# Kernel optimization log

Hardware: AMD Instinct MI355X
Metric: run time of the kernel (lower is better)

The kernel has to match this reference:

```python
import math
import jax, jax.numpy as jnp
import numpy as np

B, T, D = 512, 512, 256
ALPHA = 0.5
BETA = 0.9


def setup_inputs() -> dict:
    key = jax.random.key(0)
    ks = jax.random.split(key, 9)
    s = 1.0 / math.sqrt(D)
    return {
        "window_features": jax.random.normal(ks[0], (B, T, D), jnp.float32),
        "timestamps": jax.random.uniform(ks[1], (B, T), jnp.float32) * 86400.0 * 7,
        "prev_L": jax.random.normal(ks[2], (B, D), jnp.float32),
        "prev_M": jax.random.uniform(ks[3], (B, 1), jnp.float32),
        "pad_mask": jnp.zeros((B, T), jnp.bool_),
        "W_Q": jax.random.normal(ks[4], (D, D), jnp.float32) * s,
        "W_K": jax.random.normal(ks[5], (D, D), jnp.float32) * s,
        "W_V": jax.random.normal(ks[6], (D, D), jnp.float32) * s,
        "cls_w": jax.random.normal(ks[7], (1, 2 * D + 1), jnp.float32) * s,
        "cls_b": jnp.zeros((1,), jnp.float32),
    }


def reference(window_features, timestamps, prev_L, prev_M, pad_mask,
              W_Q, W_K, W_V, cls_w, cls_b):
    Bv, Tv, d = window_features.shape
    valid = ~pad_mask
    valid_f = valid.astype(window_features.dtype)              # [B,T]
    valid_count = jnp.clip(valid_f.sum(1, keepdims=True), 1.0)  # [B,1]

    # decay weights from recency (days)
    t_masked = jnp.where(pad_mask, -1e18, timestamps)
    t_max = t_masked.max(1, keepdims=True)                      # [B,1]
    dt = jnp.clip(t_max - timestamps, 0.0) / 86400.0
    lam = jnp.exp(-ALPHA * dt) * valid_f                        # [B,T]

    # mean-pooled query
    q = (window_features * valid_f[..., None]).sum(1) / valid_count  # [B,d]
    Q = q @ W_Q.T                                               # [B,d]
    K = jnp.einsum('btd,ed->bte', window_features, W_K)         # [B,T,d]
    V = jnp.einsum('btd,ed->bte', window_features, W_V)         # [B,T,d]

    scores = jnp.einsum('bd,btd->bt', Q, K) / math.sqrt(d)      # [B,T]
    scores = jnp.where(pad_mask, -1e9, scores)
    attn = jax.nn.softmax(scores, axis=-1)

    # decay-modulated reweighting + renormalization
    w = lam * attn
    w = w / (w.sum(1, keepdims=True) + 1e-8)

    L_t = jnp.einsum('bt,btd->bd', w, V)                        # [B,d]
    delta_t = L_t - prev_L
    M_t = BETA * prev_M + (1.0 - BETA) * jnp.linalg.norm(delta_t, axis=1, keepdims=True)
    T_event = jnp.concatenate([L_t, delta_t, M_t], axis=-1)     # [B,2d+1]
    p = (T_event @ cls_w.T + cls_b).squeeze(-1)                 # [B]
    return (p, T_event, L_t, M_t)
```

## Files before the change

kernel.cpp:

```cpp
#include <hip/hip_runtime.h>
#include <math.h>

#define ALPHA 0.5f
#define BETA 0.9f
#define Bsz 512
#define Tsz 512
#define Dsz 256

__device__ __forceinline__ float wave_reduce_sum(float v) {
    v += __shfl_xor(v, 32, 64);
    v += __shfl_xor(v, 16, 64);
    v += __shfl_xor(v, 8, 64);
    v += __shfl_xor(v, 4, 64);
    v += __shfl_xor(v, 2, 64);
    v += __shfl_xor(v, 1, 64);
    return v;
}

__device__ __forceinline__ float wave_reduce_max(float v) {
    v = fmaxf(v, __shfl_xor(v, 32, 64));
    v = fmaxf(v, __shfl_xor(v, 16, 64));
    v = fmaxf(v, __shfl_xor(v, 8, 64));
    v = fmaxf(v, __shfl_xor(v, 4, 64));
    v = fmaxf(v, __shfl_xor(v, 2, 64));
    v = fmaxf(v, __shfl_xor(v, 1, 64));
    return v;
}

__global__ __launch_bounds__(256) void kA(const float* __restrict__ x,
                                          const float* __restrict__ ts,
                                          const unsigned char* __restrict__ pad,
                                          const float* __restrict__ WQ,
                                          const float* __restrict__ WK,
                                          float* __restrict__ qk,
                                          float* __restrict__ tmax_out) {
    const int b = blockIdx.x;
    const int tid = threadIdx.x;
    const int w = tid >> 6, lane = tid & 63;

    __shared__ float validS[Tsz];
    __shared__ float qpart[4][Dsz];
    __shared__ float qS[Dsz];
    __shared__ float QS[Dsz];
    __shared__ float red[8];
    __shared__ float tmaxS, cntS;

    float lmax = -1e30f;
    float lcnt = 0.f;
    for (int t = tid; t < Tsz; t += 256) {
        bool v = (pad[(size_t)b * Tsz + t] == 0);
        float tv = ts[(size_t)b * Tsz + t];
        validS[t] = v ? 1.f : 0.f;
        if (v) { lmax = fmaxf(lmax, tv); lcnt += 1.f; }
    }
    lmax = wave_reduce_max(lmax);
    lcnt = wave_reduce_sum(lcnt);
    if (lane == 0) { red[w] = lmax; red[4 + w] = lcnt; }
    __syncthreads();
    if (tid == 0) {
        tmaxS = fmaxf(fmaxf(red[0], red[1]), fmaxf(red[2], red[3]));
        cntS = fmaxf(red[4] + red[5] + red[6] + red[7], 1.f);
    }
    __syncthreads();

    const float* xb = x + (size_t)b * Tsz * Dsz;
    float4 a0 = make_float4(0.f, 0.f, 0.f, 0.f);
    float4 a1 = a0, a2 = a0, a3 = a0;
    const int tbase = w * 128;
    for (int i = 0; i < 128; i += 4) {
        const int t = tbase + i;
        float4 x0 = *(const float4*)(xb + (size_t)(t + 0) * Dsz + lane * 4);
        float4 x1 = *(const float4*)(xb + (size_t)(t + 1) * Dsz + lane * 4);
        float4 x2 = *(const float4*)(xb + (size_t)(t + 2) * Dsz + lane * 4);
        float4 x3 = *(const float4*)(xb + (size_t)(t + 3) * Dsz + lane * 4);
        const float v0 = validS[t], v1 = validS[t + 1], v2 = validS[t + 2], v3 = validS[t + 3];
        a0.x += v0 * x0.x; a0.y += v0 * x0.y; a0.z += v0 * x0.z; a0.w += v0 * x0.w;
        a1.x += v1 * x1.x; a1.y += v1 * x1.y; a1.z += v1 * x1.z; a1.w += v1 * x1.w;
        a2.x += v2 * x2.x; a2.y += v2 * x2.y; a2.z += v2 * x2.z; a2.w += v2 * x2.w;
        a3.x += v3 * x3.x; a3.y += v3 * x3.y; a3.z += v3 * x3.z; a3.w += v3 * x3.w;
    }
    float4 accq;
    accq.x = (a0.x + a1.x) + (a2.x + a3.x);
    accq.y = (a0.y + a1.y) + (a2.y + a3.y);
    accq.z = (a0.z + a1.z) + (a2.z + a3.z);
    accq.w = (a0.w + a1.w) + (a2.w + a3.w);
    qpart[w][lane * 4 + 0] = accq.x;
    qpart[w][lane * 4 + 1] = accq.y;
    qpart[w][lane * 4 + 2] = accq.z;
    qpart[w][lane * 4 + 3] = accq.w;
    __syncthreads();
    qS[tid] = (qpart[0][tid] + qpart[1][tid] + qpart[2][tid] + qpart[3][tid]) / cntS;
    __syncthreads();

    float Qi = 0.f;
    const float* wqrow = WQ + (size_t)tid * Dsz;
    #pragma unroll 4
    for (int d4 = 0; d4 < Dsz; d4 += 4) {
        float4 wv = *(const float4*)(wqrow + d4);
        Qi += wv.x * qS[d4] + wv.y * qS[d4 + 1] + wv.z * qS[d4 + 2] + wv.w * qS[d4 + 3];
    }
    QS[tid] = Qi;
    __syncthreads();

    float v = 0.f;
    #pragma unroll 8
    for (int e = 0; e < Dsz; ++e) {
        v += QS[e] * WK[(size_t)e * Dsz + tid];
    }
    qk[(size_t)b * Dsz + tid] = v * 0.0625f;
    if (tid == 0) tmax_out[b] = tmaxS;
}

__global__ __launch_bounds__(256) void kB(const float* __restrict__ x,
                                          const float* __restrict__ ts,
                                          const unsigned char* __restrict__ pad,
                                          const float* __restrict__ qk,
                                          const float* __restrict__ tmax_in,
                                          const float* __restrict__ WV,
                                          const float* __restrict__ prevL,
                                          const float* __restrict__ prevM,
                                          const float* __restrict__ clsw,
                                          const float* __restrict__ clsb,
                                          float* __restrict__ out) {
    const int b = blockIdx.x;
    const int tid = threadIdx.x;
    const int w = tid >> 6, lane = tid & 63;

    __shared__ float lamS[Tsz];
    __shared__ float okS[Tsz];
    __shared__ float accS[4][Dsz];
    __shared__ float EGS[8];
    __shared__ float xwS[Dsz];
    __shared__ float red[4];
    __shared__ float red2[4];

    const float tmax = tmax_in[b];
    for (int t = tid; t < Tsz; t += 256) {
        bool valid = (pad[(size_t)b * Tsz + t] == 0);
        float dt = fmaxf(tmax - ts[(size_t)b * Tsz + t], 0.f) * (1.f / 86400.f);
        lamS[t] = valid ? __expf(-ALPHA * dt) : 0.f;
        okS[t] = valid ? 1.f : 0.f;
    }
    __syncthreads();

    const float4 qk4 = *(const float4*)(qk + (size_t)b * Dsz + lane * 4);
    const float* xb = x + (size_t)b * Tsz * Dsz;
    float4 acc = make_float4(0.f, 0.f, 0.f, 0.f);
    float E = 0.f, G = 0.f;
    const int tbase = w * 128;
    for (int i = 0; i < 128; i += 4) {
        const int t = tbase + i;
        float4 x0 = *(const float4*)(xb + (size_t)(t + 0) * Dsz + lane * 4);
        float4 x1 = *(const float4*)(xb + (size_t)(t + 1) * Dsz + lane * 4);
        float4 x2 = *(const float4*)(xb + (size_t)(t + 2) * Dsz + lane * 4);
        float4 x3 = *(const float4*)(xb + (size_t)(t + 3) * Dsz + lane * 4);
        float s0 = qk4.x * x0.x + qk4.y * x0.y + qk4.z * x0.z + qk4.w * x0.w;
        float s1 = qk4.x * x1.x + qk4.y * x1.y + qk4.z * x1.z + qk4.w * x1.w;
        float s2 = qk4.x * x2.x + qk4.y * x2.y + qk4.z * x2.z + qk4.w * x2.w;
        float s3 = qk4.x * x3.x + qk4.y * x3.y + qk4.z * x3.z + qk4.w * x3.w;
        #pragma unroll
        for (int off = 32; off >= 1; off >>= 1) {
            s0 += __shfl_xor(s0, off, 64);
            s1 += __shfl_xor(s1, off, 64);
            s2 += __shfl_xor(s2, off, 64);
            s3 += __shfl_xor(s3, off, 64);
        }
        float e0 = okS[t + 0] * __expf(s0);
        float e1 = okS[t + 1] * __expf(s1);
        float e2 = okS[t + 2] * __expf(s2);
        float e3 = okS[t + 3] * __expf(s3);
        float g0 = lamS[t + 0] * e0;
        float g1 = lamS[t + 1] * e1;
        float g2 = lamS[t + 2] * e2;
        float g3 = lamS[t + 3] * e3;
        E += (e0 + e1) + (e2 + e3);
        G += (g0 + g1) + (g2 + g3);
        acc.x += g0 * x0.x + g1 * x1.x + g2 * x2.x + g3 * x3.x;
        acc.y += g0 * x0.y + g1 * x1.y + g2 * x2.y + g3 * x3.y;
        acc.z += g0 * x0.z + g1 * x1.z + g2 * x2.z + g3 * x3.z;
        acc.w += g0 * x0.w + g1 * x1.w + g2 * x2.w + g3 * x3.w;
    }
    accS[w][lane * 4 + 0] = acc.x;
    accS[w][lane * 4 + 1] = acc.y;
    accS[w][lane * 4 + 2] = acc.z;
    accS[w][lane * 4 + 3] = acc.w;
    if (lane == 0) { EGS[w] = E; EGS[4 + w] = G; }
    __syncthreads();

    {
        float Et = EGS[0] + EGS[1] + EGS[2] + EGS[3];
        float Gt = EGS[4] + EGS[5] + EGS[6] + EGS[7];
        float denom = Gt + 1e-8f * Et;
        float accd = accS[0][tid] + accS[1][tid] + accS[2][tid] + accS[3][tid];
        xwS[tid] = (denom > 0.f) ? accd / denom : 0.f;
    }
    __syncthreads();

    float Le = 0.f;
    const float* wvrow = WV + (size_t)tid * Dsz;
    #pragma unroll 4
    for (int d4 = 0; d4 < Dsz; d4 += 4) {
        float4 wv = *(const float4*)(wvrow + d4);
        Le += wv.x * xwS[d4] + wv.y * xwS[d4 + 1] + wv.z * xwS[d4 + 2] + wv.w * xwS[d4 + 3];
    }
    float delta = Le - prevL[(size_t)b * Dsz + tid];

    float ssq = wave_reduce_sum(delta * delta);
    if (lane == 0) red[w] = ssq;
    __syncthreads();
    float nrm = sqrtf(red[0] + red[1] + red[2] + red[3]);
    float M = BETA * prevM[b] + (1.f - BETA) * nrm;

    float pp = Le * clsw[tid] + delta * clsw[Dsz + tid];
    float psum = wave_reduce_sum(pp);
    if (lane == 0) red2[w] = psum;
    __syncthreads();

    float* out_p = out;
    float* out_T = out + Bsz;
    float* out_L = out + Bsz + (size_t)Bsz * (2 * Dsz + 1);
    float* out_M = out + Bsz + (size_t)Bsz * (2 * Dsz + 1) + (size_t)Bsz * Dsz;

    out_T[(size_t)b * (2 * Dsz + 1) + tid] = Le;
    out_T[(size_t)b * (2 * Dsz + 1) + Dsz + tid] = delta;
    out_L[(size_t)b * Dsz + tid] = Le;
    if (tid == 0) {
        float p = red2[0] + red2[1] + red2[2] + red2[3] + M * clsw[2 * Dsz] + clsb[0];
        out_p[b] = p;
        out_T[(size_t)b * (2 * Dsz + 1) + 2 * Dsz] = M;
        out_M[b] = M;
    }
}

extern "C" void kernel_launch(void* const* d_in, const int* in_sizes, int n_in,
                              void* d_out, int out_size, void* d_ws, size_t ws_size,
                              hipStream_t stream) {
    const float* x     = (const float*)d_in[0];
    const float* ts    = (const float*)d_in[1];
    const float* prevL = (const float*)d_in[2];
    const float* prevM = (const float*)d_in[3];
    const unsigned char* pad = (const unsigned char*)d_in[4];
    const float* WQ    = (const float*)d_in[5];
    const float* WK    = (const float*)d_in[6];
    const float* WV    = (const float*)d_in[7];
    const float* clsw  = (const float*)d_in[8];
    const float* clsb  = (const float*)d_in[9];

    float* ws   = (float*)d_ws;
    float* qk   = ws;
    float* tmax = ws + Bsz * Dsz;

    kA<<<Bsz, 256, 0, stream>>>(x, ts, pad, WQ, WK, qk, tmax);
    kB<<<Bsz, 256, 0, stream>>>(x, ts, pad, qk, tmax, WV, prevL, prevM, clsw, clsb, (float*)d_out);
}
```

Before: 453.4 us.

## Double-buffer x tiles into LDS via async global_load_lds in kB

The kB main loop now streams x through LDS in double-buffered 32-row tiles using global_load_lds, so the next tile's load overlaps compute on the current one. Score dot products are split so 8 lanes share one row, which cuts the shuffle reduction from 6 steps to 3. Tiles are processed in reverse order and blocks in reverse batch order, apparently to reuse L2 lines left by kA's forward pass. The cost is 64KB of LDS per block, which lowers occupancy, plus one barrier per tile.

After: 453.3 us. About the same (-0.0%).

```diff
diff --git a/kernel.cpp b/kernel.cpp
--- a/kernel.cpp
+++ b/kernel.cpp
@@ -6,6 +6,8 @@
 #define Bsz 512
 #define Tsz 512
 #define Dsz 256
+#define TILE 32
+#define NTILE (Tsz / TILE)
 
 __device__ __forceinline__ float wave_reduce_sum(float v) {
     v += __shfl_xor(v, 32, 64);
@@ -25,6 +27,13 @@
     v = fmaxf(v, __shfl_xor(v, 2, 64));
     v = fmaxf(v, __shfl_xor(v, 1, 64));
     return v;
+}
+
+__device__ __forceinline__ void load_lds16(const float* g, float* l) {
+    __builtin_amdgcn_global_load_lds(
+        (const __attribute__((address_space(1))) void*)(g),
+        (__attribute__((address_space(3))) void*)(l),
+        16, 0, 0);
 }
 
 __global__ __launch_bounds__(256) void kA(const float* __restrict__ x,
@@ -122,12 +131,16 @@
                                           const float* __restrict__ clsw,
                                           const float* __restrict__ clsb,
                                           float* __restrict__ out) {
-    const int b = blockIdx.x;
+    const int b = (Bsz - 1) - blockIdx.x;
     const int tid = threadIdx.x;
     const int w = tid >> 6, lane = tid & 63;
-
+    const int rloc = lane >> 3;
+    const int sub = lane & 7;
+
+    __shared__ __align__(16) float buf[2][TILE][Dsz];
     __shared__ float lamS[Tsz];
     __shared__ float okS[Tsz];
+    __shared__ float gS[TILE];
     __shared__ float accS[4][Dsz];
     __shared__ float EGS[8];
     __shared__ float xwS[Dsz];
@@ -141,50 +154,75 @@
         lamS[t] = valid ? __expf(-ALPHA * dt) : 0.f;
         okS[t] = valid ? 1.f : 0.f;
     }
-    __syncthreads();
-
-    const float4 qk4 = *(const float4*)(qk + (size_t)b * Dsz + lane * 4);
+
+    float4 qkr[8];
+    #pragma unroll
+    for (int jj = 0; jj < 8; ++jj)
+        qkr[jj] = *(const float4*)(qk + (size_t)b * Dsz + ((jj * 8 + sub) << 2));
+
     const float* xb = x + (size_t)b * Tsz * Dsz;
+
+    {
+        const int t0 = (NTILE - 1) * TILE;
+        #pragma unroll
+        for (int k = 0; k < 8; ++k) {
+            const int r = w * 8 + k;
+            load_lds16(xb + (size_t)(t0 + r) * Dsz + lane * 4, &buf[0][r][0]);
+        }
+    }
+    __syncthreads();
+
     float4 acc = make_float4(0.f, 0.f, 0.f, 0.f);
     float E = 0.f, G = 0.f;
-    const int tbase = w * 128;
-    for (int i = 0; i < 128; i += 4) {
-        const int t = tbase + i;
-        float4 x0 = *(const float4*)(xb + (size_t)(t + 0) * Dsz + lane * 4);
-        float4 x1 = *(const float4*)(xb + (size_t)(t + 1) * Dsz + lane * 4);
-        float4 x2 = *(const float4*)(xb + (size_t)(t + 2) * Dsz + lane * 4);
-        float4 x3 = *(const float4*)(xb + (size_t)(t + 3) * Dsz + lane * 4);
-        float s0 = qk4.x * x0.x + qk4.y * x0.y + qk4.z * x0.z + qk4.w * x0.w;
-        float s1 = qk4.x * x1.x + qk4.y * x1.y + qk4.z * x1.z + qk4.w * x1.w;
-        float s2 = qk4.x * x2.x + qk4.y * x2.y + qk4.z * x2.z + qk4.w * x2.w;
-        float s3 = qk4.x * x3.x + qk4.y * x3.y + qk4.z * x3.z + qk4.w * x3.w;
+    int cur = 0;
+
+    for (int it = 0; it < NTILE; ++it) {
+        const int tile = (NTILE - 1) - it;
+
+        if (it + 1 < NTILE) {
+            const int t0 = (tile - 1) * TILE;
+            #pragma unroll
+            for (int k = 0; k < 8; ++k) {
+                const int r = w * 8 + k;
+                load_lds16(xb + (size_t)(t0 + r) * Dsz + lane * 4, &buf[cur ^ 1][r][0]);
+            }
+        }
+
+        const int r = w * 8 + rloc;
+        const float* rowp = &buf[cur][r][0];
+        float s = 0.f;
         #pragma unroll
-        for (int off = 32; off >= 1; off >>= 1) {
-            s0 += __shfl_xor(s0, off, 64);
-            s1 += __shfl_xor(s1, off, 64);
-            s2 += __shfl_xor(s2, off, 64);
-            s3 += __shfl_xor(s3, off, 64);
-        }
-        float e0 = okS[t + 0] * __expf(s0);
-        float e1 = okS[t + 1] * __expf(s1);
-        float e2 = okS[t + 2] * __expf(s2);
-        float e3 = okS[t + 3] * __expf(s3);
-        float g0 = lamS[t + 0] * e0;
-        float g1 = lamS[t + 1] * e1;
-        float g2 = lamS[t + 2] * e2;
-        float g3 = lamS[t + 3] * e3;
-        E += (e0 + e1) + (e2 + e3);
-        G += (g0 + g1) + (g2 + g3);
-        acc.x += g0 * x0.x + g1 * x1.x + g2 * x2.x + g3 * x3.x;
-        acc.y += g0 * x0.y + g1 * x1.y + g2 * x2.y + g3 * x3.y;
-        acc.z += g0 * x0.z + g1 * x1.z + g2 * x2.z + g3 * x3.z;
-        acc.w += g0 * x0.w + g1 * x1.w + g2 * x2.w + g3 * x3.w;
-    }
+        for (int jj = 0; jj < 8; ++jj) {
+            const float4 xv = *(const float4*)(rowp + ((jj * 8 + sub) << 2));
+            s += xv.x * qkr[jj].x + xv.y * qkr[jj].y + xv.z * qkr[jj].z + xv.w * qkr[jj].w;
+        }
+        s += __shfl_xor(s, 1, 64);
+        s += __shfl_xor(s, 2, 64);
+        s += __shfl_xor(s, 4, 64);
+        const int tglob = tile * TILE + r;
+        const float e = okS[tglob] * __expf(s);
+        const float g = lamS[tglob] * e;
+        E += e; G += g;
+        if (sub == 0) gS[r] = g;
+
+        #pragma unroll
+        for (int k = 0; k < 8; ++k) {
+            const float g_k = gS[w * 8 + k];
+            const float4 xv = *(const float4*)(&buf[cur][w * 8 + k][lane * 4]);
+            acc.x += g_k * xv.x; acc.y += g_k * xv.y; acc.z += g_k * xv.z; acc.w += g_k * xv.w;
+        }
+
+        __syncthreads();
+        cur ^= 1;
+    }
+
     accS[w][lane * 4 + 0] = acc.x;
     accS[w][lane * 4 + 1] = acc.y;
     accS[w][lane * 4 + 2] = acc.z;
     accS[w][lane * 4 + 3] = acc.w;
-    if (lane == 0) { EGS[w] = E; EGS[4 + w] = G; }
+    float Ew = wave_reduce_sum(E) * 0.125f;
+    float Gw = wave_reduce_sum(G) * 0.125f;
+    if (lane == 0) { EGS[w] = Ew; EGS[4 + w] = Gw; }
     __syncthreads();
 
     {
```
